# Performance work log

Measured on AMD Instinct MI355X. Metric: run time of the kernel, lower is better.

## Reference

```python
import jax, jax.numpy as jnp
import numpy as np

B, DIN, H, DOUT = 4096, 2048, 4096, 2048


def setup_inputs() -> dict:
    key = jax.random.key(0)
    ks = jax.random.split(key, 17)
    x = jax.random.normal(ks[0], (B, DIN), dtype=jnp.float32)
    W0 = jax.random.randint(ks[1], (H, DIN), -127, 128, dtype=jnp.int32)
    b0 = jax.random.randint(ks[2], (H,), -127, 128, dtype=jnp.int32)
    W2 = jax.random.randint(ks[3], (H, H), -127, 128, dtype=jnp.int32)
    b2 = jax.random.randint(ks[4], (H,), -127, 128, dtype=jnp.int32)
    W4 = jax.random.randint(ks[5], (DOUT, H), -127, 128, dtype=jnp.int32)
    b4 = jax.random.randint(ks[6], (DOUT,), -127, 128, dtype=jnp.int32)
    # amax scalars: positive calibration ranges in [0.5, 2.0)
    amaxes = [jax.random.uniform(ks[7 + i], (), jnp.float32, 0.5, 2.0) for i in range(9)]
    (a0_in, a0_w, a0_b, a2_in, a2_w, a2_b, a4_in, a4_w, a4_b) = amaxes
    return {"x": x, "W0": W0, "b0": b0, "W2": W2, "b2": b2, "W4": W4, "b4": b4,
            "a0_in": a0_in, "a0_w": a0_w, "a0_b": a0_b,
            "a2_in": a2_in, "a2_w": a2_w, "a2_b": a2_b,
            "a4_in": a4_in, "a4_w": a4_w, "a4_b": a4_b}


def _quant(x, amax):
    # torch: clamp(round(x * 127/amax), -127, 127).int()
    scale = 127.0 / amax
    return jnp.clip(jnp.round(x * scale), -127.0, 127.0).astype(jnp.int32)


def _layer(x, W, b, a_in, a_w, a_b):
    xq = _quant(x, a_in)                                      # [B, in] int32
    acc = jnp.matmul(xq, W.T, preferred_element_type=jnp.int32)  # [B, out] int32
    y = acc.astype(jnp.float32) * (a_w * a_in / (127.0 ** 2))    # double dequant
    return y + b.astype(jnp.float32) * (a_b / 127.0)             # single dequant bias


def reference(x, W0, b0, W2, b2, W4, b4,
              a0_in, a0_w, a0_b, a2_in, a2_w, a2_b, a4_in, a4_w, a4_b):
    x = x.reshape(x.shape[0], -1)
    x = _layer(x, W0, b0, a0_in, a0_w, a0_b)
    x = jax.nn.relu(x)
    x = _layer(x, W2, b2, a2_in, a2_w, a2_b)
    x = jax.nn.relu(x)
    x = _layer(x, W4, b4, a4_in, a4_w, a4_b)
    return x
```

## Files before the change

### kernel.cpp

```cpp
#include <hip/hip_runtime.h>

using i32x4 = __attribute__((ext_vector_type(4))) int;

#define DEVI static __device__ __forceinline__

DEVI void gload_lds16(const void* g, void* l) {
  __builtin_amdgcn_global_load_lds(
      (const __attribute__((address_space(1))) void*)g,
      (__attribute__((address_space(3))) void*)l, 16, 0, 0);
}

template <int N> DEVI void vmcnt_n() {
  asm volatile("s_waitcnt vmcnt(%0)" ::"n"(N) : "memory");
}
template <int N> DEVI void lgkm_n() {
  asm volatile("s_waitcnt lgkmcnt(%0)" ::"n"(N) : "memory");
}

#define FENCE() asm volatile("" ::: "memory")
#define BARX()                    \
  do {                            \
    FENCE();                      \
    __builtin_amdgcn_s_barrier(); \
    FENCE();                      \
  } while (0)
#define SCHB() __builtin_amdgcn_sched_barrier(0)
#define PRIO1() __builtin_amdgcn_s_setprio(1)
#define PRIO0() __builtin_amdgcn_s_setprio(0)

__global__ void __launch_bounds__(256) pack_w_kernel(const int* __restrict__ w,
                                                     signed char* __restrict__ o,
                                                     int n4) {
  int stride = gridDim.x * blockDim.x;
  for (int i = blockIdx.x * blockDim.x + threadIdx.x; i < n4; i += stride) {
    int4 v = reinterpret_cast<const int4*>(w)[i];
    char4 c;
    c.x = (signed char)v.x;
    c.y = (signed char)v.y;
    c.z = (signed char)v.z;
    c.w = (signed char)v.w;
    reinterpret_cast<char4*>(o)[i] = c;
  }
}

__global__ void __launch_bounds__(256) quant_x_kernel(const float* __restrict__ x,
                                                      signed char* __restrict__ o,
                                                      const float* __restrict__ amax,
                                                      int n4) {
  const float s = 127.0f / amax[0];
  int stride = gridDim.x * blockDim.x;
  for (int i = blockIdx.x * blockDim.x + threadIdx.x; i < n4; i += stride) {
    float4 v = reinterpret_cast<const float4*>(x)[i];
    char4 c;
    float q;
    q = fminf(fmaxf(rintf(__fmul_rn(v.x, s)), -127.0f), 127.0f); c.x = (signed char)(int)q;
    q = fminf(fmaxf(rintf(__fmul_rn(v.y, s)), -127.0f), 127.0f); c.y = (signed char)(int)q;
    q = fminf(fmaxf(rintf(__fmul_rn(v.z, s)), -127.0f), 127.0f); c.z = (signed char)(int)q;
    q = fminf(fmaxf(rintf(__fmul_rn(v.w, s)), -127.0f), 127.0f); c.w = (signed char)(int)q;
    reinterpret_cast<char4*>(o)[i] = c;
  }
}


#define STG(b, kt)                                                             \
  do {                                                                         \
    const int k0_ = (kt)*128 + scol;                                           \
    _Pragma("unroll") for (int j = 0; j < NN; ++j)                             \
        gload_lds16(Wb + (size_t)((j)*64 + srow) * K + k0_,                    \
                    &lds[b][ABYTES + (j)*8192 + tid * 16]);                    \
    gload_lds16(Ab + (size_t)(srow) * K + k0_, &lds[b][tid * 16]);             \
    gload_lds16(Ab + (size_t)(64 + srow) * K + k0_, &lds[b][8192 + tid * 16]); \
    gload_lds16(Ab + (size_t)(128 + srow) * K + k0_, &lds[b][16384 + tid * 16]); \
    gload_lds16(Ab + (size_t)(192 + srow) * K + k0_, &lds[b][24576 + tid * 16]); \
  } while (0)

#define AF_(b, m, h) \
  (*(const i32x4*)&lds[b][(wrl + (m)*16 + ro) * 128 + ((h) ? cS1 : cS0)])
#define BF_(b, n, h) \
  (*(const i32x4*)&lds[b][ABYTES + (wcl + (n)*16 + ro) * 128 + ((h) ? cS1 : cS0)])

#define RD_AF(dst, b, m0)            \
  do {                               \
    dst[0][0] = AF_(b, m0, 0);       \
    dst[0][1] = AF_(b, m0, 1);       \
    dst[1][0] = AF_(b, (m0) + 1, 0); \
    dst[1][1] = AF_(b, (m0) + 1, 1); \
  } while (0)

#define READ_BF(b)                                   \
  do {                                               \
    _Pragma("unroll") for (int n = 0; n < NN; ++n) { \
      bf[n][0] = BF_(b, n, 0);                       \
      bf[n][1] = BF_(b, n, 1);                       \
    }                                                \
  } while (0)

#define MFMA_P(mp, af)                                                                     \
  do {                                                                                     \
    _Pragma("unroll") for (int n = 0; n < NN; ++n) {                                       \
      acc[2 * (mp)][n] =                                                                   \
          __builtin_amdgcn_mfma_i32_16x16x64_i8(af[0][0], bf[n][0], acc[2 * (mp)][n], 0, 0, 0); \
      acc[2 * (mp)][n] =                                                                   \
          __builtin_amdgcn_mfma_i32_16x16x64_i8(af[0][1], bf[n][1], acc[2 * (mp)][n], 0, 0, 0); \
      acc[2 * (mp) + 1][n] = __builtin_amdgcn_mfma_i32_16x16x64_i8(                        \
          af[1][0], bf[n][0], acc[2 * (mp) + 1][n], 0, 0, 0);                              \
      acc[2 * (mp) + 1][n] = __builtin_amdgcn_mfma_i32_16x16x64_i8(                        \
          af[1][1], bf[n][1], acc[2 * (mp) + 1][n], 0, 0, 0);                              \
    }                                                                                      \
  } while (0)

#define TILE_1B(b, t)                              \
  do {                                             \
    RD_AF(afX, b, 0);                              \
    READ_BF(b);                                    \
    RD_AF(afY, b, 2);                              \
    if ((t) + 1 < nt) STG(1 - (b), (t) + 1);       \
    lgkm_n<4>(); SCHB();                           \
    PRIO1(); MFMA_P(0, afX); PRIO0();              \
    RD_AF(afX, b, 4);                              \
    lgkm_n<4>(); SCHB();                           \
    PRIO1(); MFMA_P(1, afY); PRIO0();              \
    RD_AF(afY, b, 6);                              \
    lgkm_n<4>(); SCHB();                           \
    PRIO1(); MFMA_P(2, afX); PRIO0();              \
    lgkm_n<0>(); SCHB();                           \
    PRIO1(); MFMA_P(3, afY); PRIO0();              \
    vmcnt_n<0>();                                  \
  } while (0)

template <int BN, int OUT_I8>
__global__ __launch_bounds__(512, 2) void gemm_r9_kernel(
    const signed char* __restrict__ A, const signed char* __restrict__ W,
    const int* __restrict__ bias, void* __restrict__ out, int M, int N, int K,
    const float* __restrict__ p_ain, const float* __restrict__ p_aw,
    const float* __restrict__ p_ab, const float* __restrict__ p_anext) {
  static_assert(BN == 256 || BN == 128, "");
  constexpr int NN = BN / 64;
  constexpr int ABYTES = 256 * 128;
  __shared__ signed char lds[2][ABYTES + BN * 128];

  const int tid = threadIdx.x;
  const int lane = tid & 63;
  const int wave = tid >> 6;
  const int wrl = (wave >> 2) * 128;
  const int wcl = (wave & 3) * (BN / 4);

  const int lin = blockIdx.y * gridDim.x + blockIdx.x;
  const int cpx = (gridDim.x * gridDim.y) >> 3;
  const int swz = (lin & 7) * cpx + (lin >> 3);
  const int tileM = (swz / gridDim.x) * 256;
  const int tileN = (swz % gridDim.x) * BN;

  const signed char* Ab = A + (size_t)tileM * K;
  const signed char* Wb = W + (size_t)tileN * K;

  const int srow = tid >> 3;
  const int scol = ((tid & 7) ^ (srow & 7)) * 16;

  const int ro = lane & 15;
  const int kg = lane >> 4;
  const int cS0 = ((kg ^ (ro & 7)) << 4);
  const int cS1 = (((4 + kg) ^ (ro & 7)) << 4);

  const int nt = K >> 7;

  i32x4 acc[8][NN] = {};
  i32x4 afX[2][2], afY[2][2], bf[NN][2];

  STG(0, 0);
  vmcnt_n<0>();

  for (int t = 0; t < nt; t += 2) {
    BARX();
    TILE_1B(0, t);
    BARX();
    TILE_1B(1, t + 1);
  }

  const float s1 = __fmul_rn(p_aw[0], p_ain[0]) / 16129.0f;
  const float s2 = p_ab[0] / 127.0f;
  float qs = 0.0f;
  if (OUT_I8) qs = 127.0f / p_anext[0];

#pragma unroll
  for (int m = 0; m < 8; ++m) {
#pragma unroll
    for (int n = 0; n < NN; ++n) {
      const int col = tileN + wcl + n * 16 + ro;
      const int row0 = tileM + wrl + m * 16 + kg * 4;
      const float bv = __fmul_rn((float)bias[col], s2);
#pragma unroll
      for (int i = 0; i < 4; ++i) {
        float y = __fadd_rn(__fmul_rn((float)acc[m][n][i], s1), bv);
        if (OUT_I8) {
          float rl = fmaxf(y, 0.0f);
          float q = fminf(rintf(__fmul_rn(rl, qs)), 127.0f);
          ((signed char*)out)[(size_t)(row0 + i) * N + col] = (signed char)(int)q;
        } else {
          ((float*)out)[(size_t)(row0 + i) * N + col] = y;
        }
      }
    }
  }
}

extern "C" void kernel_launch(void* const* d_in, const int* in_sizes, int n_in,
                              void* d_out, int out_size, void* d_ws, size_t ws_size,
                              hipStream_t stream) {
  const float* x = (const float*)d_in[0];
  const int* W0 = (const int*)d_in[1];
  const int* b0 = (const int*)d_in[2];
  const int* W2 = (const int*)d_in[3];
  const int* b2 = (const int*)d_in[4];
  const int* W4 = (const int*)d_in[5];
  const int* b4 = (const int*)d_in[6];
  const float* a0_in = (const float*)d_in[7];
  const float* a0_w = (const float*)d_in[8];
  const float* a0_b = (const float*)d_in[9];
  const float* a2_in = (const float*)d_in[10];
  const float* a2_w = (const float*)d_in[11];
  const float* a2_b = (const float*)d_in[12];
  const float* a4_in = (const float*)d_in[13];
  const float* a4_w = (const float*)d_in[14];
  const float* a4_b = (const float*)d_in[15];

  constexpr int Bb = 4096, DIN = 2048, H = 4096, DOUT = 2048;
  constexpr size_t MB = 1u << 20;

  char* ws = (char*)d_ws;
  signed char* xq0 = (signed char*)(ws);
  signed char* xq2 = (signed char*)(ws);
  signed char* W0q = (signed char*)(ws + 8 * MB);
  signed char* W2q = (signed char*)(ws + 16 * MB);
  signed char* W4q = (signed char*)(ws + 32 * MB);
  signed char* xq1 = (signed char*)(ws + 40 * MB);

  pack_w_kernel<<<2048, 256, 0, stream>>>(W0, W0q, H * DIN / 4);
  pack_w_kernel<<<2048, 256, 0, stream>>>(W2, W2q, H * H / 4);
  pack_w_kernel<<<2048, 256, 0, stream>>>(W4, W4q, DOUT * H / 4);
  quant_x_kernel<<<2048, 256, 0, stream>>>(x, xq0, a0_in, Bb * DIN / 4);

  gemm_r9_kernel<256, 1><<<dim3(H / 256, Bb / 256), 512, 0, stream>>>(
      xq0, W0q, b0, xq1, Bb, H, DIN, a0_in, a0_w, a0_b, a2_in);
  gemm_r9_kernel<256, 1><<<dim3(H / 256, Bb / 256), 512, 0, stream>>>(
      xq1, W2q, b2, xq2, Bb, H, H, a2_in, a2_w, a2_b, a4_in);
  gemm_r9_kernel<128, 0><<<dim3(DOUT / 128, Bb / 256), 512, 0, stream>>>(
      xq2, W4q, b4, d_out, Bb, DOUT, H, a4_in, a4_w, a4_b, a4_in);
}
```

Measured before the change: 162.1 us.

## Pre-pack weights into MFMA fragment layout and load B directly to registers

The weight packing kernel now writes int8 weights in MFMA fragment order (16 columns by 64 k per 1 KB block). The GEMM then loads B operands straight from global memory into registers with double-buffered register sets, skipping LDS staging for W. This cuts LDS footprint and traffic for B and drops the B LDS reads. In exchange, each wave fetches its own B fragments from global or L2 with no sharing through LDS across the two row-waves, and register pressure rises.

```diff
diff --git a/kernel.cpp b/kernel.cpp
--- a/kernel.cpp
+++ b/kernel.cpp
@@ -28,18 +28,28 @@
 #define PRIO1() __builtin_amdgcn_s_setprio(1)
 #define PRIO0() __builtin_amdgcn_s_setprio(0)
 
-__global__ void __launch_bounds__(256) pack_w_kernel(const int* __restrict__ w,
-                                                     signed char* __restrict__ o,
-                                                     int n4) {
+DEVI unsigned pk4(const int* s) {
+  return (unsigned)(unsigned char)s[0] | ((unsigned)(unsigned char)s[1] << 8) |
+         ((unsigned)(unsigned char)s[2] << 16) |
+         ((unsigned)(unsigned char)s[3] << 24);
+}
+
+__global__ void __launch_bounds__(256) pack_wfrag_kernel(
+    const int* __restrict__ w, signed char* __restrict__ o, int K, int nchunks) {
+  const int KB = K >> 6;
   int stride = gridDim.x * blockDim.x;
-  for (int i = blockIdx.x * blockDim.x + threadIdx.x; i < n4; i += stride) {
-    int4 v = reinterpret_cast<const int4*>(w)[i];
-    char4 c;
-    c.x = (signed char)v.x;
-    c.y = (signed char)v.y;
-    c.z = (signed char)v.z;
-    c.w = (signed char)v.w;
-    reinterpret_cast<char4*>(o)[i] = c;
+  for (int i = blockIdx.x * blockDim.x + threadIdx.x; i < nchunks; i += stride) {
+    const int b = i >> 6, l = i & 63;
+    const int cblk = b / KB, kblk = b - cblk * KB;
+    const int c = cblk * 16 + (l & 15);
+    const int k0 = kblk * 64 + (l >> 4) * 16;
+    const int* src = w + (size_t)c * K + k0;
+    int4 v;
+    v.x = (int)pk4(src);
+    v.y = (int)pk4(src + 4);
+    v.z = (int)pk4(src + 8);
+    v.w = (int)pk4(src + 12);
+    *reinterpret_cast<int4*>(o + (size_t)i * 16) = v;
   }
 }
 
@@ -62,22 +72,17 @@
 }
 
 
-#define STG(b, kt)                                                             \
-  do {                                                                         \
-    const int k0_ = (kt)*128 + scol;                                           \
-    _Pragma("unroll") for (int j = 0; j < NN; ++j)                             \
-        gload_lds16(Wb + (size_t)((j)*64 + srow) * K + k0_,                    \
-                    &lds[b][ABYTES + (j)*8192 + tid * 16]);                    \
-    gload_lds16(Ab + (size_t)(srow) * K + k0_, &lds[b][tid * 16]);             \
-    gload_lds16(Ab + (size_t)(64 + srow) * K + k0_, &lds[b][8192 + tid * 16]); \
+#define STG(b, kt)                                                               \
+  do {                                                                           \
+    const int k0_ = (kt)*128 + scol;                                             \
+    gload_lds16(Ab + (size_t)(srow) * K + k0_, &lds[b][tid * 16]);               \
+    gload_lds16(Ab + (size_t)(64 + srow) * K + k0_, &lds[b][8192 + tid * 16]);   \
     gload_lds16(Ab + (size_t)(128 + srow) * K + k0_, &lds[b][16384 + tid * 16]); \
     gload_lds16(Ab + (size_t)(192 + srow) * K + k0_, &lds[b][24576 + tid * 16]); \
   } while (0)
 
 #define AF_(b, m, h) \
   (*(const i32x4*)&lds[b][(wrl + (m)*16 + ro) * 128 + ((h) ? cS1 : cS0)])
-#define BF_(b, n, h) \
-  (*(const i32x4*)&lds[b][ABYTES + (wcl + (n)*16 + ro) * 128 + ((h) ? cS1 : cS0)])
 
 #define RD_AF(dst, b, m0)            \
   do {                               \
@@ -87,57 +92,58 @@
     dst[1][1] = AF_(b, (m0) + 1, 1); \
   } while (0)
 
-#define READ_BF(b)                                   \
-  do {                                               \
-    _Pragma("unroll") for (int n = 0; n < NN; ++n) { \
-      bf[n][0] = BF_(b, n, 0);                       \
-      bf[n][1] = BF_(b, n, 1);                       \
-    }                                                \
-  } while (0)
-
-#define MFMA_P(mp, af)                                                                     \
+#define LD_BF(dst, t)                                                           \
+  do {                                                                          \
+    _Pragma("unroll") for (int n = 0; n < NN; ++n) {                            \
+      dst[n][0] = *(const i32x4*)(Wpw + ((size_t)(n)*KB + 2 * (t)) * 1024);     \
+      dst[n][1] = *(const i32x4*)(Wpw + ((size_t)(n)*KB + 2 * (t) + 1) * 1024); \
+    }                                                                           \
+  } while (0)
+
+#define MFMA_P(mp, af, bfc)                                                                \
   do {                                                                                     \
     _Pragma("unroll") for (int n = 0; n < NN; ++n) {                                       \
-      acc[2 * (mp)][n] =                                                                   \
-          __builtin_amdgcn_mfma_i32_16x16x64_i8(af[0][0], bf[n][0], acc[2 * (mp)][n], 0, 0, 0); \
-      acc[2 * (mp)][n] =                                                                   \
-          __builtin_amdgcn_mfma_i32_16x16x64_i8(af[0][1], bf[n][1], acc[2 * (mp)][n], 0, 0, 0); \
+      acc[2 * (mp)][n] = __builtin_amdgcn_mfma_i32_16x16x64_i8(af[0][0], bfc[n][0],        \
+                                                               acc[2 * (mp)][n], 0, 0, 0); \
+      acc[2 * (mp)][n] = __builtin_amdgcn_mfma_i32_16x16x64_i8(af[0][1], bfc[n][1],        \
+                                                               acc[2 * (mp)][n], 0, 0, 0); \
       acc[2 * (mp) + 1][n] = __builtin_amdgcn_mfma_i32_16x16x64_i8(                        \
-          af[1][0], bf[n][0], acc[2 * (mp) + 1][n], 0, 0, 0);                              \
+          af[1][0], bfc[n][0], acc[2 * (mp) + 1][n], 0, 0, 0);                             \
       acc[2 * (mp) + 1][n] = __builtin_amdgcn_mfma_i32_16x16x64_i8(                        \
-          af[1][1], bf[n][1], acc[2 * (mp) + 1][n], 0, 0, 0);                              \
+          af[1][1], bfc[n][1], acc[2 * (mp) + 1][n], 0, 0, 0);                             \
     }                                                                                      \
   } while (0)
 
-#define TILE_1B(b, t)                              \
+#define TILE_R10(b, t, bfC, bfN)                   \
   do {                                             \
     RD_AF(afX, b, 0);                              \
-    READ_BF(b);                                    \
     RD_AF(afY, b, 2);                              \
-    if ((t) + 1 < nt) STG(1 - (b), (t) + 1);       \
+    if ((t) + 1 < nt) {                            \
+      STG(1 - (b), (t) + 1);                       \
+      LD_BF(bfN, (t) + 1);                         \
+    }                                              \
     lgkm_n<4>(); SCHB();                           \
-    PRIO1(); MFMA_P(0, afX); PRIO0();              \
+    PRIO1(); MFMA_P(0, afX, bfC); PRIO0();         \
     RD_AF(afX, b, 4);                              \
     lgkm_n<4>(); SCHB();                           \
-    PRIO1(); MFMA_P(1, afY); PRIO0();              \
+    PRIO1(); MFMA_P(1, afY, bfC); PRIO0();         \
     RD_AF(afY, b, 6);                              \
     lgkm_n<4>(); SCHB();                           \
-    PRIO1(); MFMA_P(2, afX); PRIO0();              \
+    PRIO1(); MFMA_P(2, afX, bfC); PRIO0();         \
     lgkm_n<0>(); SCHB();                           \
-    PRIO1(); MFMA_P(3, afY); PRIO0();              \
+    PRIO1(); MFMA_P(3, afY, bfC); PRIO0();         \
     vmcnt_n<0>();                                  \
   } while (0)
 
 template <int BN, int OUT_I8>
-__global__ __launch_bounds__(512, 2) void gemm_r9_kernel(
-    const signed char* __restrict__ A, const signed char* __restrict__ W,
+__global__ __launch_bounds__(512, 2) void gemm_r10_kernel(
+    const signed char* __restrict__ A, const signed char* __restrict__ Wp,
     const int* __restrict__ bias, void* __restrict__ out, int M, int N, int K,
     const float* __restrict__ p_ain, const float* __restrict__ p_aw,
     const float* __restrict__ p_ab, const float* __restrict__ p_anext) {
   static_assert(BN == 256 || BN == 128, "");
   constexpr int NN = BN / 64;
-  constexpr int ABYTES = 256 * 128;
-  __shared__ signed char lds[2][ABYTES + BN * 128];
+  __shared__ signed char lds[2][256 * 128];
 
   const int tid = threadIdx.x;
   const int lane = tid & 63;
@@ -152,7 +158,6 @@
   const int tileN = (swz % gridDim.x) * BN;
 
   const signed char* Ab = A + (size_t)tileM * K;
-  const signed char* Wb = W + (size_t)tileN * K;
 
   const int srow = tid >> 3;
   const int scol = ((tid & 7) ^ (srow & 7)) * 16;
@@ -162,19 +167,24 @@
   const int cS0 = ((kg ^ (ro & 7)) << 4);
   const int cS1 = (((4 + kg) ^ (ro & 7)) << 4);
 
+  const int KB = K >> 6;
+  const signed char* Wpw =
+      Wp + ((size_t)((tileN + wcl) >> 4) * KB) * 1024 + (size_t)lane * 16;
+
   const int nt = K >> 7;
 
   i32x4 acc[8][NN] = {};
-  i32x4 afX[2][2], afY[2][2], bf[NN][2];
+  i32x4 afX[2][2], afY[2][2], bf0[NN][2], bf1[NN][2];
 
   STG(0, 0);
+  LD_BF(bf0, 0);
   vmcnt_n<0>();
 
   for (int t = 0; t < nt; t += 2) {
     BARX();
-    TILE_1B(0, t);
+    TILE_R10(0, t, bf0, bf1);
     BARX();
-    TILE_1B(1, t + 1);
+    TILE_R10(1, t + 1, bf1, bf0);
   }
 
   const float s1 = __fmul_rn(p_aw[0], p_ain[0]) / 16129.0f;
@@ -235,15 +245,15 @@
   signed char* W4q = (signed char*)(ws + 32 * MB);
   signed char* xq1 = (signed char*)(ws + 40 * MB);
 
-  pack_w_kernel<<<2048, 256, 0, stream>>>(W0, W0q, H * DIN / 4);
-  pack_w_kernel<<<2048, 256, 0, stream>>>(W2, W2q, H * H / 4);
-  pack_w_kernel<<<2048, 256, 0, stream>>>(W4, W4q, DOUT * H / 4);
+  pack_wfrag_kernel<<<2048, 256, 0, stream>>>(W0, W0q, DIN, H * DIN / 16);
+  pack_wfrag_kernel<<<2048, 256, 0, stream>>>(W2, W2q, H, H * H / 16);
+  pack_wfrag_kernel<<<2048, 256, 0, stream>>>(W4, W4q, H, DOUT * H / 16);
   quant_x_kernel<<<2048, 256, 0, stream>>>(x, xq0, a0_in, Bb * DIN / 4);
 
-  gemm_r9_kernel<256, 1><<<dim3(H / 256, Bb / 256), 512, 0, stream>>>(
+  gemm_r10_kernel<256, 1><<<dim3(H / 256, Bb / 256), 512, 0, stream>>>(
       xq0, W0q, b0, xq1, Bb, H, DIN, a0_in, a0_w, a0_b, a2_in);
-  gemm_r9_kernel<256, 1><<<dim3(H / 256, Bb / 256), 512, 0, stream>>>(
+  gemm_r10_kernel<256, 1><<<dim3(H / 256, Bb / 256), 512, 0, stream>>>(
       xq1, W2q, b2, xq2, Bb, H, H, a2_in, a2_w, a2_b, a4_in);
-  gemm_r9_kernel<128, 0><<<dim3(DOUT / 128, Bb / 256), 512, 0, stream>>>(
+  gemm_r10_kernel<128, 0><<<dim3(DOUT / 128, Bb / 256), 512, 0, stream>>>(
       xq2, W4q, b4, d_out, Bb, DOUT, H, a4_in, a4_w, a4_b, a4_in);
 }
```

New measurement: 212.4 us. 1.31x slower.

## Merge prep kernels and fold next-layer weight packing into GEMM epilogues

Applied to the files above, without the earlier changes.

The W0 packing and x quantisation kernels become one prep launch. Packing of W2 and W4 now runs as a tail loop inside the preceding GEMM kernels, after their epilogue. This removes three kernel launches and lets the packing traffic reuse GEMM blocks instead of separate grids. In exchange, the GEMM blocks do extra memory-bound work at their end, which lengthens the tail of each GEMM.

```diff
diff --git a/kernel.cpp b/kernel.cpp
--- a/kernel.cpp
+++ b/kernel.cpp
@@ -28,48 +28,45 @@
 #define PRIO1() __builtin_amdgcn_s_setprio(1)
 #define PRIO0() __builtin_amdgcn_s_setprio(0)
 
-__global__ void __launch_bounds__(256) pack_w_kernel(const int* __restrict__ w,
-                                                     signed char* __restrict__ o,
-                                                     int n4) {
+__global__ void __launch_bounds__(256) prep_kernel(
+    const int* __restrict__ W0, const float* __restrict__ x,
+    const float* __restrict__ amax, signed char* __restrict__ W0q,
+    signed char* __restrict__ xq, int c0, int cx) {
+  const float s = 127.0f / amax[0];
+  const int total = c0 + cx;
   int stride = gridDim.x * blockDim.x;
-  for (int i = blockIdx.x * blockDim.x + threadIdx.x; i < n4; i += stride) {
-    int4 v = reinterpret_cast<const int4*>(w)[i];
-    char4 c;
-    c.x = (signed char)v.x;
-    c.y = (signed char)v.y;
-    c.z = (signed char)v.z;
-    c.w = (signed char)v.w;
-    reinterpret_cast<char4*>(o)[i] = c;
-  }
-}
-
-__global__ void __launch_bounds__(256) quant_x_kernel(const float* __restrict__ x,
-                                                      signed char* __restrict__ o,
-                                                      const float* __restrict__ amax,
-                                                      int n4) {
-  const float s = 127.0f / amax[0];
-  int stride = gridDim.x * blockDim.x;
-  for (int i = blockIdx.x * blockDim.x + threadIdx.x; i < n4; i += stride) {
-    float4 v = reinterpret_cast<const float4*>(x)[i];
-    char4 c;
-    float q;
-    q = fminf(fmaxf(rintf(__fmul_rn(v.x, s)), -127.0f), 127.0f); c.x = (signed char)(int)q;
-    q = fminf(fmaxf(rintf(__fmul_rn(v.y, s)), -127.0f), 127.0f); c.y = (signed char)(int)q;
-    q = fminf(fmaxf(rintf(__fmul_rn(v.z, s)), -127.0f), 127.0f); c.z = (signed char)(int)q;
-    q = fminf(fmaxf(rintf(__fmul_rn(v.w, s)), -127.0f), 127.0f); c.w = (signed char)(int)q;
-    reinterpret_cast<char4*>(o)[i] = c;
-  }
-}
-
-
-#define STG(b, kt)                                                             \
-  do {                                                                         \
-    const int k0_ = (kt)*128 + scol;                                           \
-    _Pragma("unroll") for (int j = 0; j < NN; ++j)                             \
-        gload_lds16(Wb + (size_t)((j)*64 + srow) * K + k0_,                    \
-                    &lds[b][ABYTES + (j)*8192 + tid * 16]);                    \
-    gload_lds16(Ab + (size_t)(srow) * K + k0_, &lds[b][tid * 16]);             \
-    gload_lds16(Ab + (size_t)(64 + srow) * K + k0_, &lds[b][8192 + tid * 16]); \
+  for (int i = blockIdx.x * blockDim.x + threadIdx.x; i < total; i += stride) {
+    if (i < c0) {
+      int4 v = reinterpret_cast<const int4*>(W0)[i];
+      char4 c;
+      c.x = (signed char)v.x;
+      c.y = (signed char)v.y;
+      c.z = (signed char)v.z;
+      c.w = (signed char)v.w;
+      reinterpret_cast<char4*>(W0q)[i] = c;
+    } else {
+      int j = i - c0;
+      float4 v = reinterpret_cast<const float4*>(x)[j];
+      char4 c;
+      float q;
+      q = fminf(fmaxf(rintf(__fmul_rn(v.x, s)), -127.0f), 127.0f); c.x = (signed char)(int)q;
+      q = fminf(fmaxf(rintf(__fmul_rn(v.y, s)), -127.0f), 127.0f); c.y = (signed char)(int)q;
+      q = fminf(fmaxf(rintf(__fmul_rn(v.z, s)), -127.0f), 127.0f); c.z = (signed char)(int)q;
+      q = fminf(fmaxf(rintf(__fmul_rn(v.w, s)), -127.0f), 127.0f); c.w = (signed char)(int)q;
+      reinterpret_cast<char4*>(xq)[j] = c;
+    }
+  }
+}
+
+
+#define STG(b, kt)                                                               \
+  do {                                                                           \
+    const int k0_ = (kt)*128 + scol;                                             \
+    _Pragma("unroll") for (int j = 0; j < NN; ++j)                               \
+        gload_lds16(Wb + (size_t)((j)*64 + srow) * K + k0_,                      \
+                    &lds[b][ABYTES + (j)*8192 + tid * 16]);                      \
+    gload_lds16(Ab + (size_t)(srow) * K + k0_, &lds[b][tid * 16]);               \
+    gload_lds16(Ab + (size_t)(64 + srow) * K + k0_, &lds[b][8192 + tid * 16]);   \
     gload_lds16(Ab + (size_t)(128 + srow) * K + k0_, &lds[b][16384 + tid * 16]); \
     gload_lds16(Ab + (size_t)(192 + srow) * K + k0_, &lds[b][24576 + tid * 16]); \
   } while (0)
@@ -129,11 +126,12 @@
   } while (0)
 
 template <int BN, int OUT_I8>
-__global__ __launch_bounds__(512, 2) void gemm_r9_kernel(
+__global__ __launch_bounds__(512, 2) void gemm_r13_kernel(
     const signed char* __restrict__ A, const signed char* __restrict__ W,
     const int* __restrict__ bias, void* __restrict__ out, int M, int N, int K,
     const float* __restrict__ p_ain, const float* __restrict__ p_aw,
-    const float* __restrict__ p_ab, const float* __restrict__ p_anext) {
+    const float* __restrict__ p_ab, const float* __restrict__ p_anext,
+    const int* __restrict__ pw, signed char* __restrict__ po, int pn4) {
   static_assert(BN == 256 || BN == 128, "");
   constexpr int NN = BN / 64;
   constexpr int ABYTES = 256 * 128;
@@ -202,6 +200,20 @@
       }
     }
   }
+
+  if (pw != nullptr) {
+    const int nblk = gridDim.x * gridDim.y;
+    const int stride = nblk * 512;
+    for (int i = lin * 512 + tid; i < pn4; i += stride) {
+      int4 v = reinterpret_cast<const int4*>(pw)[i];
+      char4 c;
+      c.x = (signed char)v.x;
+      c.y = (signed char)v.y;
+      c.z = (signed char)v.z;
+      c.w = (signed char)v.w;
+      reinterpret_cast<char4*>(po)[i] = c;
+    }
+  }
 }
 
 extern "C" void kernel_launch(void* const* d_in, const int* in_sizes, int n_in,
@@ -235,15 +247,16 @@
   signed char* W4q = (signed char*)(ws + 32 * MB);
   signed char* xq1 = (signed char*)(ws + 40 * MB);
 
-  pack_w_kernel<<<2048, 256, 0, stream>>>(W0, W0q, H * DIN / 4);
-  pack_w_kernel<<<2048, 256, 0, stream>>>(W2, W2q, H * H / 4);
-  pack_w_kernel<<<2048, 256, 0, stream>>>(W4, W4q, DOUT * H / 4);
-  quant_x_kernel<<<2048, 256, 0, stream>>>(x, xq0, a0_in, Bb * DIN / 4);
-
-  gemm_r9_kernel<256, 1><<<dim3(H / 256, Bb / 256), 512, 0, stream>>>(
-      xq0, W0q, b0, xq1, Bb, H, DIN, a0_in, a0_w, a0_b, a2_in);
-  gemm_r9_kernel<256, 1><<<dim3(H / 256, Bb / 256), 512, 0, stream>>>(
-      xq1, W2q, b2, xq2, Bb, H, H, a2_in, a2_w, a2_b, a4_in);
-  gemm_r9_kernel<128, 0><<<dim3(DOUT / 128, Bb / 256), 512, 0, stream>>>(
-      xq2, W4q, b4, d_out, Bb, DOUT, H, a4_in, a4_w, a4_b, a4_in);
-}
+  prep_kernel<<<2048, 256, 0, stream>>>(W0, x, a0_in, W0q, xq0, H * DIN / 4,
+                                        Bb * DIN / 4);
+
+  gemm_r13_kernel<256, 1><<<dim3(H / 256, Bb / 256), 512, 0, stream>>>(
+      xq0, W0q, b0, xq1, Bb, H, DIN, a0_in, a0_w, a0_b, a2_in,
+      W2, W2q, H * H / 4);
+  gemm_r13_kernel<256, 1><<<dim3(H / 256, Bb / 256), 512, 0, stream>>>(
+      xq1, W2q, b2, xq2, Bb, H, H, a2_in, a2_w, a2_b, a4_in,
+      W4, W4q, DOUT * H / 4);
+  gemm_r13_kernel<128, 0><<<dim3(DOUT / 128, Bb / 256), 512, 0, stream>>>(
+      xq2, W4q, b4, d_out, Bb, DOUT, H, a4_in, a4_w, a4_b, a4_in,
+      nullptr, nullptr, 0);
+}
```

Result: slower. 166.1 us (+2.5%).
